# Kernel tuning notes

Hardware: AMD Instinct MI355X
Metric: run time of the kernel (lower is better)

## Reference

```python
import jax, jax.numpy as jnp
import numpy as np
import math

NUM_LEAD = 12
PATCHES = 100  # patch_num_v * patch_num_h = 5 * 20
HEADS = 12
HID = 768
DH = HID // HEADS  # 64
SEQ = NUM_LEAD * PATCHES + NUM_LEAD + 1  # 1213
INTER = 3072
BATCH = 8


def _layer_norm(x, g, b, eps=1e-12):
    u = x.mean(-1, keepdims=True)
    s = ((x - u) ** 2).mean(-1, keepdims=True)
    return g * (x - u) / jnp.sqrt(s + eps) + b


def _lead_mask():
    # make_mask with fusion == 0: additive bias applied to query rows [0, NUM_LEAD+1)
    cols = jnp.arange(SEQ)
    # CLS row: 1 at lead-token positions 1..NUM_LEAD
    cls_row = jnp.where((cols >= 1) & (cols < NUM_LEAD + 1), 1.0, 0.0)
    # Lead rows: 1 everywhere except own patch block
    i = jnp.arange(NUM_LEAD)[:, None]
    start = NUM_LEAD + 1 + PATCHES * i
    in_block = (cols[None, :] >= start) & (cols[None, :] < start + PATCHES)
    lead_rows = jnp.where(in_block, 0.0, 1.0)
    mask = jnp.concatenate([cls_row[None, :], lead_rows], axis=0)  # [NUM_LEAD+1, SEQ]
    return mask * (-99999.0)


def setup_inputs() -> dict:
    key = jax.random.key(0)
    ks = jax.random.split(key, 12)
    std = 0.02
    d = {
        "hidden_states": jax.random.normal(ks[0], (BATCH, SEQ, HID), jnp.float32),
        "attention_mask": jnp.zeros((BATCH, 1, 1, SEQ), jnp.float32),
        "Wq": jax.random.normal(ks[1], (HID, HID), jnp.float32) * std,
        "bq": jnp.zeros((HID,), jnp.float32),
        "Wk": jax.random.normal(ks[2], (HID, HID), jnp.float32) * std,
        "bk": jnp.zeros((HID,), jnp.float32),
        "Wv": jax.random.normal(ks[3], (HID, HID), jnp.float32) * std,
        "bv": jnp.zeros((HID,), jnp.float32),
        "Wo": jax.random.normal(ks[4], (HID, HID), jnp.float32) * std,
        "bo": jnp.zeros((HID,), jnp.float32),
        "gamma1": jnp.ones((HID,), jnp.float32),
        "beta1": jnp.zeros((HID,), jnp.float32),
        "Wi": jax.random.normal(ks[5], (HID, INTER), jnp.float32) * std,
        "bi": jnp.zeros((INTER,), jnp.float32),
        "Wd": jax.random.normal(ks[6], (INTER, HID), jnp.float32) * std,
        "bd": jnp.zeros((HID,), jnp.float32),
        "gamma2": jnp.ones((HID,), jnp.float32),
        "beta2": jnp.zeros((HID,), jnp.float32),
    }
    return d


def reference(hidden_states, attention_mask, Wq, bq, Wk, bk, Wv, bv, Wo, bo,
              gamma1, beta1, Wi, bi, Wd, bd, gamma2, beta2):
    B, S, _ = hidden_states.shape

    def heads(x):  # [B,S,HID] -> [B,H,S,DH]
        return x.reshape(B, S, HEADS, DH).transpose(0, 2, 1, 3)

    q = heads(hidden_states @ Wq + bq)
    k = heads(hidden_states @ Wk + bk)
    v = heads(hidden_states @ Wv + bv)

    scores = jnp.einsum("bhqd,bhkd->bhqk", q, k) / math.sqrt(DH)
    scores = scores + attention_mask  # broadcast [B,1,1,S]
    lead_mask = _lead_mask()  # [NUM_LEAD+1, SEQ]
    scores = scores.at[:, :, : NUM_LEAD + 1, :].add(lead_mask[None, None])

    probs = jax.nn.softmax(scores, axis=-1)  # dropout is identity in eval
    ctx = jnp.einsum("bhqk,bhkd->bhqd", probs, v)
    ctx = ctx.transpose(0, 2, 1, 3).reshape(B, S, HID)

    attn_out = _layer_norm(ctx @ Wo + bo + hidden_states, gamma1, beta1)
    inter = jax.nn.gelu(attn_out @ Wi + bi, approximate=False)  # exact erf gelu
    out = _layer_norm(inter @ Wd + bd + attn_out, gamma2, beta2)
    return out
```

## Files before the change

kernel.cpp:

```cpp
#include <hip/hip_runtime.h>
#include <hip/hip_bf16.h>
#include <stdint.h>

typedef unsigned short u16;
typedef unsigned int u32;
typedef __attribute__((ext_vector_type(8))) short frag8;
typedef __attribute__((ext_vector_type(4))) float f32x4;

#define SEQ 1213
#define BATCH 8
#define HEADS 12
#define DH 64
#define HID 768
#define INTER 3072
#define BS (BATCH*SEQ)
#define LOG2E 1.44269504088896f

#define MFMA(a,b,c) __builtin_amdgcn_mfma_f32_16x16x32_bf16(a,b,c,0,0,0)

__device__ __forceinline__ float b2f(u16 u){ u32 i=((u32)u)<<16; float f; __builtin_memcpy(&f,&i,4); return f; }
__device__ __forceinline__ u16 f2b(float f){ u32 i; __builtin_memcpy(&i,&f,4); i = i + 0x7fffu + ((i>>16)&1u); return (u16)(i>>16); }
__device__ __forceinline__ u32 pack2(float a, float b){ return (u32)f2b(a) | ((u32)f2b(b)<<16); }

__device__ __forceinline__ void async16(const u16* g, u16* l){
  __builtin_amdgcn_global_load_lds((const __attribute__((address_space(1))) u32*)(uintptr_t)g,
                                   (__attribute__((address_space(3))) u32*)(uintptr_t)l, 16, 0, 0);
}

__global__ __launch_bounds__(256) void convert_arr(const void* __restrict__ src,
  u16* __restrict__ dst, int n8, const u16* __restrict__ probe)
{
  const bool f32 = (probe[0] == 0);
  int i = blockIdx.x*256 + threadIdx.x;
  if (i >= n8) return;
  u16 tmp[8];
  if (f32){
    const float* s = (const float*)src + (size_t)i*8;
#pragma unroll
    for (int j=0;j<8;j++) tmp[j] = f2b(s[j]);
  } else {
    *(uint4*)tmp = *((const uint4*)src + i);
  }
  *((uint4*)dst + i) = *(const uint4*)tmp;
}

__global__ __launch_bounds__(256) void convert_small(
  const void* bq, const void* bk, const void* bv, const void* bo,
  const void* bi, const void* bd, const void* g1, const void* be1,
  const void* g2, const void* be2, const void* am,
  u16* __restrict__ dst, const u16* __restrict__ probe)
{
  const int starts[12] = {0,768,1536,2304,3072,6144,6912,7680,8448,9216,9984,19688};
  const void* srcs[11] = {bq,bk,bv,bo,bi,bd,g1,be1,g2,be2,am};
  const bool f32 = (probe[0] == 0);
  int e = (blockIdx.x*256 + threadIdx.x) * 8;
  if (e >= 19688) return;
  int seg = 0;
#pragma unroll
  for (int k=1;k<11;k++) if (starts[k] <= e) seg = k;
  int off = e - starts[seg];
  const void* s = srcs[seg];
  u16 tmp[8];
  if (f32){
    const float* sf = (const float*)s + off;
#pragma unroll
    for (int j=0;j<8;j++) tmp[j] = f2b(sf[j]);
  } else {
    const u16* sh = (const u16*)s + off;
#pragma unroll
    for (int j=0;j<8;j++) tmp[j] = sh[j];
  }
  *(uint4*)(dst + e) = *(const uint4*)tmp;
}

__global__ __launch_bounds__(256) void transpose2(const void* __restrict__ in,
  u16* __restrict__ out, int R, int C, const u16* __restrict__ probe)
{
  const bool f32 = (probe[0] == 0);
  __shared__ u16 tile[32][33];
  const int bx = blockIdx.x*32, by = blockIdx.y*32;
  const int tx = threadIdx.x & 31, ty = threadIdx.x >> 5;
  if (f32){
    const float* inf_ = (const float*)in;
#pragma unroll
    for (int i=ty;i<32;i+=8) tile[i][tx] = f2b(inf_[(size_t)(by+i)*C + bx+tx]);
  } else {
    const u16* inh = (const u16*)in;
#pragma unroll
    for (int i=ty;i<32;i+=8) tile[i][tx] = inh[(size_t)(by+i)*C + bx+tx];
  }
  __syncthreads();
#pragma unroll
  for (int i=ty;i<32;i+=8) out[(size_t)(bx+i)*R + by+tx] = tile[tx][i];
}

__device__ __forceinline__ void gemm_tile(
    const u16* __restrict__ A, const u16* __restrict__ BT,
    int M, int K, int m0, int n0,
    u16* ldsA, u16* ldsB, f32x4 acc[4][4])
{
  const int t = threadIdx.x;
  const int w = t >> 6, l = t & 63;
  const int lw = l & 15, lh = l >> 4;
  const int rowo = (w >> 1) << 6;
  const int colo = (w & 1) << 6;
  const int srow = w*8 + (l>>3);
  const int scol = ((l&7) ^ ((l>>3)&7)) * 8;

  const u16* gpA[4]; const u16* gpB[4];
  u16* lpA[4]; u16* lpB[4];
#pragma unroll
  for (int p=0;p<4;p++){
    int ra = m0 + p*32 + srow; if (ra >= M) ra = M-1;
    gpA[p] = A  + (size_t)ra*K + scol;
    gpB[p] = BT + (size_t)(n0 + p*32 + srow)*K + scol;
    lpA[p] = ldsA + (p*32 + w*8)*64 + l*8;
    lpB[p] = ldsB + (p*32 + w*8)*64 + l*8;
  }

  const int slot0 = lw & 7;
  for (int k0 = 0; k0 < K; k0 += 64) {
    __syncthreads();
#pragma unroll
    for (int p=0;p<4;p++) async16(gpA[p] + k0, lpA[p]);
#pragma unroll
    for (int p=0;p<4;p++) async16(gpB[p] + k0, lpB[p]);
    __syncthreads();
#pragma unroll
    for (int kk=0;kk<2;kk++){
      const int slot = ((kk*4 + lh) ^ slot0) * 8;
      frag8 af[4], bf[4];
#pragma unroll
      for (int mi=0;mi<4;mi++) af[mi] = *(const frag8*)(ldsA + (rowo + mi*16 + lw)*64 + slot);
#pragma unroll
      for (int ni=0;ni<4;ni++) bf[ni] = *(const frag8*)(ldsB + (colo + ni*16 + lw)*64 + slot);
#pragma unroll
      for (int mi=0;mi<4;mi++)
#pragma unroll
        for (int ni=0;ni<4;ni++)
          acc[mi][ni] = MFMA(af[mi], bf[ni], acc[mi][ni]);
    }
  }
}

__global__ __launch_bounds__(256,2) void gemm_qkv(
  const u16* __restrict__ A, const u16* __restrict__ BT,
  const u16* __restrict__ bq, const u16* __restrict__ bk, const u16* __restrict__ bv,
  u16* __restrict__ Qo, u16* __restrict__ Ko, u16* __restrict__ Vo)
{
  __shared__ __align__(16) u16 ldsA[128*64];
  __shared__ __align__(16) u16 ldsB[128*64];
  f32x4 acc[4][4];
#pragma unroll
  for (int i=0;i<4;i++)
#pragma unroll
    for (int j=0;j<4;j++) acc[i][j] = 0.f;
  const int m0 = blockIdx.x*128, n0 = blockIdx.y*128;
  gemm_tile(A, BT, BS, HID, m0, n0, ldsA, ldsB, acc);
  const int t=threadIdx.x, w=t>>6, l=t&63, lw=l&15, lh=l>>4;
  const int rowb = m0 + ((w>>1)<<6), colb = n0 + ((w&1)<<6);
#pragma unroll
  for (int ni=0;ni<4;ni++){
    int cc = colb + ni*16 + lw;
    int which = cc / HID;
    int n2 = cc - which*HID;
    int h = n2 >> 6, d = n2 & 63;
    const u16* bp = which==0 ? bq : (which==1 ? bk : bv);
    u16* op = which==0 ? Qo : (which==1 ? Ko : Vo);
    float bias = b2f(bp[n2]);
    float scale = which==0 ? 0.125f : 1.0f;
#pragma unroll
    for (int mi=0;mi<4;mi++){
#pragma unroll
      for (int r=0;r<4;r++){
        int rr = rowb + mi*16 + lh*4 + r;
        if (rr < BS){
          int bi_ = rr / SEQ;
          int si  = rr - bi_*SEQ;
          float v = (acc[mi][ni][r] + bias) * scale;
          op[(((size_t)(bi_*HEADS + h))*SEQ + si)*64 + d] = f2b(v);
        }
      }
    }
  }
}

__global__ __launch_bounds__(256,2) void gemm_resid(
  const u16* __restrict__ A, const u16* __restrict__ BT,
  const u16* __restrict__ bias, const u16* __restrict__ resid,
  u16* __restrict__ out, int N, int K)
{
  __shared__ __align__(16) u16 ldsA[128*64];
  __shared__ __align__(16) u16 ldsB[128*64];
  f32x4 acc[4][4];
#pragma unroll
  for (int i=0;i<4;i++)
#pragma unroll
    for (int j=0;j<4;j++) acc[i][j] = 0.f;
  const int m0 = blockIdx.x*128, n0 = blockIdx.y*128;
  gemm_tile(A, BT, BS, K, m0, n0, ldsA, ldsB, acc);
  const int t=threadIdx.x, w=t>>6, l=t&63, lw=l&15, lh=l>>4;
  const int rowb = m0 + ((w>>1)<<6), colb = n0 + ((w&1)<<6);
#pragma unroll
  for (int ni=0;ni<4;ni++){
    int cc = colb + ni*16 + lw;
    float bv_ = b2f(bias[cc]);
#pragma unroll
    for (int mi=0;mi<4;mi++){
#pragma unroll
      for (int r=0;r<4;r++){
        int rr = rowb + mi*16 + lh*4 + r;
        if (rr < BS){
          float v = acc[mi][ni][r] + bv_ + b2f(resid[(size_t)rr*N + cc]);
          out[(size_t)rr*N + cc] = f2b(v);
        }
      }
    }
  }
}

__global__ __launch_bounds__(256,2) void gemm_gelu(
  const u16* __restrict__ A, const u16* __restrict__ BT,
  const u16* __restrict__ bias, u16* __restrict__ out, int N, int K)
{
  __shared__ __align__(16) u16 ldsA[128*64];
  __shared__ __align__(16) u16 ldsB[128*64];
  f32x4 acc[4][4];
#pragma unroll
  for (int i=0;i<4;i++)
#pragma unroll
    for (int j=0;j<4;j++) acc[i][j] = 0.f;
  const int m0 = blockIdx.x*128, n0 = blockIdx.y*128;
  gemm_tile(A, BT, BS, K, m0, n0, ldsA, ldsB, acc);
  const int t=threadIdx.x, w=t>>6, l=t&63, lw=l&15, lh=l>>4;
  const int rowb = m0 + ((w>>1)<<6), colb = n0 + ((w&1)<<6);
#pragma unroll
  for (int ni=0;ni<4;ni++){
    int cc = colb + ni*16 + lw;
    float bv_ = b2f(bias[cc]);
#pragma unroll
    for (int mi=0;mi<4;mi++){
#pragma unroll
      for (int r=0;r<4;r++){
        int rr = rowb + mi*16 + lh*4 + r;
        if (rr < BS){
          float v = acc[mi][ni][r] + bv_;
          v = 0.5f * v * (1.0f + erff(v * 0.70710678118654752f));
          out[(size_t)rr*N + cc] = f2b(v);
        }
      }
    }
  }
}

__global__ __launch_bounds__(512,1) void attn_kernel(
  const u16* __restrict__ Qb, const u16* __restrict__ Kb, const u16* __restrict__ Vb,
  const u16* __restrict__ amask, u16* __restrict__ ctx)
{
  __shared__ __align__(16) u16 sQP[128*72];
  __shared__ __align__(16) u16 sK[64*72];
  __shared__ __align__(16) u16 sV[64*72];
  __shared__ float sEm[64];
  const int t = threadIdx.x, w = t>>6, l = t&63, lw = l&15, lh = l>>4;
  const int bh = blockIdx.y, b = bh / HEADS;
  const int q0 = blockIdx.x * 128;
  const int h = bh % HEADS;
  const size_t hb = (size_t)bh * SEQ * 64;
  const u16* Qp = Qb + hb;
  const u16* Kp = Kb + hb;
  const u16* Vp = Vb + hb;

  {
    int r = t >> 3, c = t & 7;
#pragma unroll
    for (int i=0;i<2;i++){
      int rr = i*64 + r;
      int s = q0 + rr; if (s > SEQ-1) s = SEQ-1;
      *(uint4*)(sQP + rr*72 + c*8) = *(const uint4*)(Qp + (size_t)s*64 + c*8);
    }
  }
  __syncthreads();
  frag8 qa[2];
#pragma unroll
  for (int kk=0;kk<2;kk++) qa[kk] = *(const frag8*)(sQP + (w*16 + lw)*72 + kk*32 + lh*8);
  u16* pw = sQP + w*16*72;

  float l_p = 0.f;
  f32x4 o[4];
#pragma unroll
  for (int i=0;i<4;i++) o[i] = 0.f;
  const bool leadwave = (q0 == 0) && (w == 0);

  const int rr = t >> 3, c = t & 7;
  const int scol = (((rr>>3) ^ (c&3))<<3) + (rr&7);

  uint4 kreg, vreg; float emreg = 0.f;
  {
    int s = rr; if (s > SEQ-1) s = SEQ-1;
    kreg = *(const uint4*)(Kp + (size_t)s*64 + c*8);
    vreg = *(const uint4*)(Vp + (size_t)s*64 + c*8);
    if (t < 64) emreg = b2f(amask[b*SEQ + t]) * LOG2E;
  }

  const int nkt = (SEQ + 63) / 64;
  for (int kt = 0; kt < nkt; kt++) {
    __syncthreads();
    {
      *(uint4*)(sK + rr*72 + c*8) = kreg;
      const u16* vp = (const u16*)&vreg;
#pragma unroll
      for (int j=0;j<8;j++)
        sV[(c*8 + j)*72 + scol] = vp[j];
      if (t < 64) sEm[t] = emreg;
    }
    __syncthreads();
    if (kt+1 < nkt){
      int s = (kt+1)*64 + rr; if (s > SEQ-1) s = SEQ-1;
      kreg = *(const uint4*)(Kp + (size_t)s*64 + c*8);
      vreg = *(const uint4*)(Vp + (size_t)s*64 + c*8);
      if (t < 64){
        int sg = (kt+1)*64 + t;
        emreg = (sg < SEQ) ? b2f(amask[b*SEQ + sg]) * LOG2E : -1e30f;
      }
    }

    f32x4 st[4];
#pragma unroll
    for (int si=0;si<4;si++){
      f32x4 a0 = 0.f;
#pragma unroll
      for (int kk=0;kk<2;kk++){
        frag8 kf = *(const frag8*)(sK + (si*16 + lw)*72 + kk*32 + lh*8);
        a0 = MFMA(kf, qa[kk], a0);
      }
      st[si] = a0;
    }

#pragma unroll
    for (int si=0;si<4;si++){
      f32x4 emv = *(const f32x4*)(sEm + si*16 + lh*4);
#pragma unroll
      for (int r=0;r<4;r++)
        st[si][r] = exp2f(fmaf(st[si][r], LOG2E, emv[r]));
    }
    if (leadwave){
#pragma unroll
      for (int si=0;si<4;si++){
#pragma unroll
        for (int r=0;r<4;r++){
          int sg = kt*64 + si*16 + lh*4 + r;
          int q = lw;
          float p = st[si][r];
          if (q == 0){
            if (sg >= 1 && sg < 13) p = 0.f;
          } else if (q < 13){
            int stt = 13 + 100*(q-1);
            if (!(sg >= stt && sg < stt+100)) p = 0.f;
          }
          st[si][r] = p;
        }
      }
    }
#pragma unroll
    for (int si=0;si<4;si++)
#pragma unroll
      for (int r=0;r<4;r++) l_p += st[si][r];

#pragma unroll
    for (int si=0;si<4;si++){
      *(u32*)(pw + lw*72 + si*16 + lh*4)     = pack2(st[si][0], st[si][1]);
      *(u32*)(pw + lw*72 + si*16 + lh*4 + 2) = pack2(st[si][2], st[si][3]);
    }
    __threadfence_block();

#pragma unroll
    for (int kk=0;kk<2;kk++){
      frag8 pf = *(const frag8*)(pw + lw*72 + kk*32 + lh*8);
#pragma unroll
      for (int ni=0;ni<4;ni++){
        int d = ni*16 + lw;
        int grp = (kk*4 + lh) ^ ((d>>3) & 3);
        frag8 vf = *(const frag8*)(sV + d*72 + (grp<<3));
        o[ni] = MFMA(pf, vf, o[ni]);
      }
    }
  }

  l_p += __shfl_xor(l_p, 16);
  l_p += __shfl_xor(l_p, 32);

#pragma unroll
  for (int r=0;r<4;r++){
    float lf = __shfl(l_p, (l & 48) + ((l >> 4) << 2) + r);
    int qg = q0 + w*16 + lh*4 + r;
    if (qg < SEQ){
      float inv = 1.0f / lf;
#pragma unroll
      for (int ni=0;ni<4;ni++){
        ctx[((size_t)(b*SEQ) + qg)*HID + h*64 + ni*16 + lw] = f2b(o[ni][r] * inv);
      }
    }
  }
}

__global__ __launch_bounds__(256) void ln_kernel(const u16* __restrict__ y,
  const u16* __restrict__ g, const u16* __restrict__ be,
  u16* __restrict__ outb, float* __restrict__ outf)
{
  const int row = blockIdx.x, t = threadIdx.x;
  const u16* yp = y + (size_t)row*HID;
  float x0 = b2f(yp[t]), x1 = b2f(yp[t+256]), x2 = b2f(yp[t+512]);
  float s = x0 + x1 + x2;
  __shared__ float red[4];
#pragma unroll
  for (int off=1; off<64; off<<=1) s += __shfl_xor(s, off);
  if ((t & 63) == 0) red[t>>6] = s;
  __syncthreads();
  float u = (red[0]+red[1]+red[2]+red[3]) * (1.0f/768.0f);
  float d0=x0-u, d1=x1-u, d2=x2-u;
  float s2 = d0*d0 + d1*d1 + d2*d2;
  __syncthreads();
#pragma unroll
  for (int off=1; off<64; off<<=1) s2 += __shfl_xor(s2, off);
  if ((t & 63) == 0) red[t>>6] = s2;
  __syncthreads();
  float var = (red[0]+red[1]+red[2]+red[3]) * (1.0f/768.0f);
  float rstd = rsqrtf(var + 1e-12f);
  float v0 = b2f(g[t])    *(d0*rstd) + b2f(be[t]);
  float v1 = b2f(g[t+256])*(d1*rstd) + b2f(be[t+256]);
  float v2 = b2f(g[t+512])*(d2*rstd) + b2f(be[t+512]);
  if (outf){
    float* op = outf + (size_t)row*HID;
    op[t] = v0; op[t+256] = v1; op[t+512] = v2;
  } else {
    u16* op = outb + (size_t)row*HID;
    op[t] = f2b(v0); op[t+256] = f2b(v1); op[t+512] = f2b(v2);
  }
}

extern "C" void kernel_launch(void* const* d_in, const int* in_sizes, int n_in,
                              void* d_out, int out_size, void* d_ws, size_t ws_size,
                              hipStream_t stream)
{
  const void* hidden = d_in[0];
  const void* amask  = d_in[1];
  const void* Wq = d_in[2];  const void* bq = d_in[3];
  const void* Wk = d_in[4];  const void* bk = d_in[5];
  const void* Wv = d_in[6];  const void* bv = d_in[7];
  const void* Wo = d_in[8];  const void* bo = d_in[9];
  const void* g1 = d_in[10]; const void* be1= d_in[11];
  const void* Wi = d_in[12]; const void* bi = d_in[13];
  const void* Wd = d_in[14]; const void* bd = d_in[15];
  const void* g2 = d_in[16]; const void* be2= d_in[17];
  const u16* probe = (const u16*)g1;

  char* ws = (char*)d_ws;
  size_t off = 0;
  auto alloc = [&](size_t elems)->u16* {
    u16* p = (u16*)(ws + off);
    off += ((elems*2 + 255) & ~(size_t)255);
    return p;
  };
  u16* hiddenC = alloc((size_t)BS*HID);
  u16* smallC  = alloc((size_t)19688);
  u16* WqkvT = alloc((size_t)2304*768);
  u16* WoT   = alloc((size_t)768*768);
  u16* WiT   = alloc((size_t)3072*768);
  u16* WdT   = alloc((size_t)768*3072);
  u16* Qb    = alloc((size_t)BS*HID);
  u16* Kb    = alloc((size_t)BS*HID);
  u16* Vb    = alloc((size_t)BS*HID);
  u16* y1    = alloc((size_t)BS*HID);
  u16* interb = Qb;
  u16* ctxb  = alloc((size_t)BS*HID);
  u16* attn_out = alloc((size_t)BS*HID);
  u16* y2 = ctxb;

  const u16* c_bq = smallC;        const u16* c_bk = smallC+768;
  const u16* c_bv = smallC+1536;   const u16* c_bo = smallC+2304;
  const u16* c_bi = smallC+3072;   const u16* c_bd = smallC+6144;
  const u16* c_g1 = smallC+6912;   const u16* c_be1= smallC+7680;
  const u16* c_g2 = smallC+8448;   const u16* c_be2= smallC+9216;
  const u16* c_am = smallC+9984;

  dim3 blk(256);
  convert_arr<<<dim3((BS*HID/8 + 255)/256), blk, 0, stream>>>(hidden, hiddenC, BS*HID/8, probe);
  convert_small<<<dim3(10), blk, 0, stream>>>(bq,bk,bv,bo,bi,bd,g1,be1,g2,be2,amask, smallC, probe);
  transpose2<<<dim3(24,24),blk,0,stream>>>(Wq, WqkvT,              768, 768, probe);
  transpose2<<<dim3(24,24),blk,0,stream>>>(Wk, WqkvT + 768*768,    768, 768, probe);
  transpose2<<<dim3(24,24),blk,0,stream>>>(Wv, WqkvT + 2*768*768,  768, 768, probe);
  transpose2<<<dim3(24,24),blk,0,stream>>>(Wo, WoT, 768, 768, probe);
  transpose2<<<dim3(96,24),blk,0,stream>>>(Wi, WiT, 768, 3072, probe);
  transpose2<<<dim3(24,96),blk,0,stream>>>(Wd, WdT, 3072, 768, probe);

  gemm_qkv<<<dim3(76,18),blk,0,stream>>>(hiddenC, WqkvT, c_bq,c_bk,c_bv, Qb,Kb,Vb);
  attn_kernel<<<dim3(10,96),dim3(512),0,stream>>>(Qb,Kb,Vb, c_am, ctxb);
  gemm_resid<<<dim3(76,6),blk,0,stream>>>(ctxb, WoT, c_bo, hiddenC, y1, 768, 768);
  ln_kernel<<<dim3(BS),blk,0,stream>>>(y1, c_g1, c_be1, attn_out, nullptr);
  gemm_gelu<<<dim3(76,24),blk,0,stream>>>(attn_out, WiT, c_bi, interb, 3072, 768);
  gemm_resid<<<dim3(76,6),blk,0,stream>>>(interb, WdT, c_bd, attn_out, y2, 768, 3072);
  ln_kernel<<<dim3(BS),blk,0,stream>>>(y2, c_g2, c_be2, nullptr, (float*)d_out);
}
```

Before: 488.9 us.

## Double-buffer LDS in GEMM and attention loops, use hardware bf16 pack

The shared GEMM tile loop now keeps two LDS stages. It prefetches the next K-slice with async global-to-LDS loads while computing on the current one, which drops one barrier per iteration. The attention kernel double-buffers its K, V and mask tiles to remove the leading barrier, and widens the V transpose swizzle from 4 to 8 groups to cut LDS bank conflicts. The bf16 pair pack uses the hardware convert instruction when the compiler provides it. LDS per GEMM block doubles to 64KB, which can limit occupancy.

After: 509.4 us. 1.04x slower.

```diff
diff --git a/kernel.cpp b/kernel.cpp
--- a/kernel.cpp
+++ b/kernel.cpp
@@ -20,7 +20,15 @@
 
 __device__ __forceinline__ float b2f(u16 u){ u32 i=((u32)u)<<16; float f; __builtin_memcpy(&f,&i,4); return f; }
 __device__ __forceinline__ u16 f2b(float f){ u32 i; __builtin_memcpy(&i,&f,4); i = i + 0x7fffu + ((i>>16)&1u); return (u16)(i>>16); }
+
+#if __has_builtin(__builtin_amdgcn_cvt_pk_bf16_f32)
+__device__ __forceinline__ u32 pack2(float a, float b){
+  auto r = __builtin_amdgcn_cvt_pk_bf16_f32(a, b);
+  u32 x; __builtin_memcpy(&x, &r, 4); return x;
+}
+#else
 __device__ __forceinline__ u32 pack2(float a, float b){ return (u32)f2b(a) | ((u32)f2b(b)<<16); }
+#endif
 
 __device__ __forceinline__ void async16(const u16* g, u16* l){
   __builtin_amdgcn_global_load_lds((const __attribute__((address_space(1))) u32*)(uintptr_t)g,
@@ -33,11 +41,11 @@
   const bool f32 = (probe[0] == 0);
   int i = blockIdx.x*256 + threadIdx.x;
   if (i >= n8) return;
-  u16 tmp[8];
+  u32 tmp[4];
   if (f32){
     const float* s = (const float*)src + (size_t)i*8;
 #pragma unroll
-    for (int j=0;j<8;j++) tmp[j] = f2b(s[j]);
+    for (int j=0;j<4;j++) tmp[j] = pack2(s[2*j], s[2*j+1]);
   } else {
     *(uint4*)tmp = *((const uint4*)src + i);
   }
@@ -118,28 +126,40 @@
     lpB[p] = ldsB + (p*32 + w*8)*64 + l*8;
   }
 
+#pragma unroll
+  for (int p=0;p<4;p++) async16(gpA[p], lpA[p]);
+#pragma unroll
+  for (int p=0;p<4;p++) async16(gpB[p], lpB[p]);
+
   const int slot0 = lw & 7;
+  int cur = 0;
   for (int k0 = 0; k0 < K; k0 += 64) {
     __syncthreads();
-#pragma unroll
-    for (int p=0;p<4;p++) async16(gpA[p] + k0, lpA[p]);
-#pragma unroll
-    for (int p=0;p<4;p++) async16(gpB[p] + k0, lpB[p]);
-    __syncthreads();
+    const int nxt = cur ^ 1;
+    if (k0 + 64 < K){
+      const int bo_ = nxt * (128*64);
+#pragma unroll
+      for (int p=0;p<4;p++) async16(gpA[p] + k0 + 64, lpA[p] + bo_);
+#pragma unroll
+      for (int p=0;p<4;p++) async16(gpB[p] + k0 + 64, lpB[p] + bo_);
+    }
+    const u16* rA = ldsA + cur*(128*64);
+    const u16* rB = ldsB + cur*(128*64);
 #pragma unroll
     for (int kk=0;kk<2;kk++){
       const int slot = ((kk*4 + lh) ^ slot0) * 8;
       frag8 af[4], bf[4];
 #pragma unroll
-      for (int mi=0;mi<4;mi++) af[mi] = *(const frag8*)(ldsA + (rowo + mi*16 + lw)*64 + slot);
-#pragma unroll
-      for (int ni=0;ni<4;ni++) bf[ni] = *(const frag8*)(ldsB + (colo + ni*16 + lw)*64 + slot);
+      for (int mi=0;mi<4;mi++) af[mi] = *(const frag8*)(rA + (rowo + mi*16 + lw)*64 + slot);
+#pragma unroll
+      for (int ni=0;ni<4;ni++) bf[ni] = *(const frag8*)(rB + (colo + ni*16 + lw)*64 + slot);
 #pragma unroll
       for (int mi=0;mi<4;mi++)
 #pragma unroll
         for (int ni=0;ni<4;ni++)
           acc[mi][ni] = MFMA(af[mi], bf[ni], acc[mi][ni]);
     }
+    cur = nxt;
   }
 }
 
@@ -148,15 +168,15 @@
   const u16* __restrict__ bq, const u16* __restrict__ bk, const u16* __restrict__ bv,
   u16* __restrict__ Qo, u16* __restrict__ Ko, u16* __restrict__ Vo)
 {
-  __shared__ __align__(16) u16 ldsA[128*64];
-  __shared__ __align__(16) u16 ldsB[128*64];
+  __shared__ __align__(16) u16 ldsA[2][128*64];
+  __shared__ __align__(16) u16 ldsB[2][128*64];
   f32x4 acc[4][4];
 #pragma unroll
   for (int i=0;i<4;i++)
 #pragma unroll
     for (int j=0;j<4;j++) acc[i][j] = 0.f;
   const int m0 = blockIdx.x*128, n0 = blockIdx.y*128;
-  gemm_tile(A, BT, BS, HID, m0, n0, ldsA, ldsB, acc);
+  gemm_tile(A, BT, BS, HID, m0, n0, &ldsA[0][0], &ldsB[0][0], acc);
   const int t=threadIdx.x, w=t>>6, l=t&63, lw=l&15, lh=l>>4;
   const int rowb = m0 + ((w>>1)<<6), colb = n0 + ((w&1)<<6);
 #pragma unroll
@@ -190,15 +210,15 @@
   const u16* __restrict__ bias, const u16* __restrict__ resid,
   u16* __restrict__ out, int N, int K)
 {
-  __shared__ __align__(16) u16 ldsA[128*64];
-  __shared__ __align__(16) u16 ldsB[128*64];
+  __shared__ __align__(16) u16 ldsA[2][128*64];
+  __shared__ __align__(16) u16 ldsB[2][128*64];
   f32x4 acc[4][4];
 #pragma unroll
   for (int i=0;i<4;i++)
 #pragma unroll
     for (int j=0;j<4;j++) acc[i][j] = 0.f;
   const int m0 = blockIdx.x*128, n0 = blockIdx.y*128;
-  gemm_tile(A, BT, BS, K, m0, n0, ldsA, ldsB, acc);
+  gemm_tile(A, BT, BS, K, m0, n0, &ldsA[0][0], &ldsB[0][0], acc);
   const int t=threadIdx.x, w=t>>6, l=t&63, lw=l&15, lh=l>>4;
   const int rowb = m0 + ((w>>1)<<6), colb = n0 + ((w&1)<<6);
 #pragma unroll
@@ -223,15 +243,15 @@
   const u16* __restrict__ A, const u16* __restrict__ BT,
   const u16* __restrict__ bias, u16* __restrict__ out, int N, int K)
 {
-  __shared__ __align__(16) u16 ldsA[128*64];
-  __shared__ __align__(16) u16 ldsB[128*64];
+  __shared__ __align__(16) u16 ldsA[2][128*64];
+  __shared__ __align__(16) u16 ldsB[2][128*64];
   f32x4 acc[4][4];
 #pragma unroll
   for (int i=0;i<4;i++)
 #pragma unroll
     for (int j=0;j<4;j++) acc[i][j] = 0.f;
   const int m0 = blockIdx.x*128, n0 = blockIdx.y*128;
-  gemm_tile(A, BT, BS, K, m0, n0, ldsA, ldsB, acc);
+  gemm_tile(A, BT, BS, K, m0, n0, &ldsA[0][0], &ldsB[0][0], acc);
   const int t=threadIdx.x, w=t>>6, l=t&63, lw=l&15, lh=l>>4;
   const int rowb = m0 + ((w>>1)<<6), colb = n0 + ((w&1)<<6);
 #pragma unroll
@@ -258,9 +278,9 @@
   const u16* __restrict__ amask, u16* __restrict__ ctx)
 {
   __shared__ __align__(16) u16 sQP[128*72];
-  __shared__ __align__(16) u16 sK[64*72];
-  __shared__ __align__(16) u16 sV[64*72];
-  __shared__ float sEm[64];
+  __shared__ __align__(16) u16 sK[2][64*72];
+  __shared__ __align__(16) u16 sV[2][64*72];
+  __shared__ float sEm[2][64];
   const int t = threadIdx.x, w = t>>6, l = t&63, lw = l&15, lh = l>>4;
   const int bh = blockIdx.y, b = bh / HEADS;
   const int q0 = blockIdx.x * 128;
@@ -292,7 +312,7 @@
   const bool leadwave = (q0 == 0) && (w == 0);
 
   const int rr = t >> 3, c = t & 7;
-  const int scol = (((rr>>3) ^ (c&3))<<3) + (rr&7);
+  const int scol = (((rr>>3) ^ c)<<3) + (rr&7);
 
   uint4 kreg, vreg; float emreg = 0.f;
   {
@@ -304,14 +324,15 @@
 
   const int nkt = (SEQ + 63) / 64;
   for (int kt = 0; kt < nkt; kt++) {
-    __syncthreads();
+    const int buf = kt & 1;
     {
-      *(uint4*)(sK + rr*72 + c*8) = kreg;
+      u16* dK = sK[buf]; u16* dV = sV[buf];
+      *(uint4*)(dK + rr*72 + c*8) = kreg;
       const u16* vp = (const u16*)&vreg;
 #pragma unroll
       for (int j=0;j<8;j++)
-        sV[(c*8 + j)*72 + scol] = vp[j];
-      if (t < 64) sEm[t] = emreg;
+        dV[(c*8 + j)*72 + scol] = vp[j];
+      if (t < 64) sEm[buf][t] = emreg;
     }
     __syncthreads();
     if (kt+1 < nkt){
@@ -324,13 +345,17 @@
       }
     }
 
+    const u16* rK = sK[buf];
+    const u16* rV = sV[buf];
+    const float* rE = sEm[buf];
+
     f32x4 st[4];
 #pragma unroll
     for (int si=0;si<4;si++){
       f32x4 a0 = 0.f;
 #pragma unroll
       for (int kk=0;kk<2;kk++){
-        frag8 kf = *(const frag8*)(sK + (si*16 + lw)*72 + kk*32 + lh*8);
+        frag8 kf = *(const frag8*)(rK + (si*16 + lw)*72 + kk*32 + lh*8);
         a0 = MFMA(kf, qa[kk], a0);
       }
       st[si] = a0;
@@ -338,7 +363,7 @@
 
 #pragma unroll
     for (int si=0;si<4;si++){
-      f32x4 emv = *(const f32x4*)(sEm + si*16 + lh*4);
+      f32x4 emv = *(const f32x4*)(rE + si*16 + lh*4);
 #pragma unroll
       for (int r=0;r<4;r++)
         st[si][r] = exp2f(fmaf(st[si][r], LOG2E, emv[r]));
@@ -379,8 +404,8 @@
 #pragma unroll
       for (int ni=0;ni<4;ni++){
         int d = ni*16 + lw;
-        int grp = (kk*4 + lh) ^ ((d>>3) & 3);
-        frag8 vf = *(const frag8*)(sV + d*72 + (grp<<3));
+        int grp = (kk*4 + lh) ^ ((d>>3) & 7);
+        frag8 vf = *(const frag8*)(rV + d*72 + (grp<<3));
         o[ni] = MFMA(pf, vf, o[ni]);
       }
     }
```
